# Performance work log

Measured on AMD Instinct MI355X. Metric: run time of the kernel, lower is better.

The kernel has to match this reference:

```python
import jax, jax.numpy as jnp
import numpy as np


def setup_inputs() -> dict:
    key = jax.random.key(0)
    k1, k2, k3 = jax.random.split(key, 3)
    B, F, D = 8192, 4096, 1024
    x = jax.random.normal(k1, (B, D), dtype=jnp.float32)
    mu = jax.random.normal(k2, (F, D), dtype=jnp.float32)
    # keep scales strictly positive and well-conditioned
    scale_diag = jax.random.uniform(k3, (F, D), dtype=jnp.float32, minval=0.5, maxval=1.5)
    return {"x": x, "mu": mu, "scale_diag": scale_diag}


def reference(x, mu, scale_diag):
    # Unnormalized diag-Gaussian log prob for every (batch, feature) pair:
    #   out[b, f] = sum_d -0.5 * ((x[b,d] - mu[f,d]) / scale[f,d])^2
    # Expanded to GEMM form (quadratic expansion):
    #   -0.5 * ( x^2 @ inv2.T  -  2 * x @ (mu*inv2).T  +  sum_d mu^2*inv2 )
    inv2 = 1.0 / (scale_diag * scale_diag)            # [F, D]
    xx = jnp.matmul(x * x, inv2.T)                    # [B, F]
    xm = jnp.matmul(x, (mu * inv2).T)                 # [B, F]
    mm = jnp.sum(mu * mu * inv2, axis=-1)             # [F]
    return -0.5 * (xx - 2.0 * xm + mm[None, :])       # [B, F]
```

## Files before the change

### kernel.cpp

```cpp
#include <hip/hip_runtime.h>
#include <hip/hip_bf16.h>
#include <cstdint>

#define B_SZ 8192
#define F_SZ 4096
#define D_SZ 1024
#define K_SZ 2048

typedef __bf16 bf16x8 __attribute__((ext_vector_type(8)));
typedef float f32x4 __attribute__((ext_vector_type(4)));
typedef float fvec4 __attribute__((ext_vector_type(4)));
typedef unsigned short u16x4 __attribute__((ext_vector_type(4)));

__device__ __forceinline__ unsigned short f2bf(float f) {
    union { float f; unsigned u; } c; c.f = f;
    unsigned r = c.u + 0x7fff + ((c.u >> 16) & 1);
    return (unsigned short)(r >> 16);
}

__device__ __forceinline__ void async16(const void* g, void* l) {
    __builtin_amdgcn_global_load_lds(
        (__attribute__((address_space(1))) void*)g,
        (__attribute__((address_space(3))) void*)l, 16, 0, 0);
}

__global__ __launch_bounds__(256) void prep(const float* __restrict__ x,
                                            const float* __restrict__ mu,
                                            const float* __restrict__ sd,
                                            unsigned short* __restrict__ A,
                                            unsigned short* __restrict__ W,
                                            float* __restrict__ nmm) {
    const int tid = threadIdx.x;
    if (blockIdx.x < 4096) {
        const size_t o0 = (size_t)blockIdx.x * 2048 + tid * 4;
        fvec4 v0 = *(const fvec4*)(x + o0);
        fvec4 v1 = *(const fvec4*)(x + o0 + 1024);
        #pragma unroll
        for (int h = 0; h < 2; ++h) {
            fvec4 v = h ? v1 : v0;
            size_t oo = o0 + h * 1024;
            size_t b = oo >> 10;
            int d = (int)(oo & 1023);
            u16x4 xx, xs;
            xx.x = f2bf(v.x * v.x); xx.y = f2bf(v.y * v.y);
            xx.z = f2bf(v.z * v.z); xx.w = f2bf(v.w * v.w);
            xs.x = f2bf(v.x); xs.y = f2bf(v.y);
            xs.z = f2bf(v.z); xs.w = f2bf(v.w);
            *(u16x4*)(A + b * K_SZ + d) = xx;
            *(u16x4*)(A + b * K_SZ + 1024 + d) = xs;
        }
    } else {
        const int f = blockIdx.x - 4096;
        const int d = tid * 4;
        size_t off = (size_t)f * D_SZ + d;
        fvec4 m = *(const fvec4*)(mu + off);
        fvec4 s = *(const fvec4*)(sd + off);
        float i0 = 1.0f / (s.x * s.x), i1 = 1.0f / (s.y * s.y);
        float i2 = 1.0f / (s.z * s.z), i3 = 1.0f / (s.w * s.w);
        u16x4 wi, wm;
        wi.x = f2bf(i0); wi.y = f2bf(i1); wi.z = f2bf(i2); wi.w = f2bf(i3);
        wm.x = f2bf(-2.0f * m.x * i0); wm.y = f2bf(-2.0f * m.y * i1);
        wm.z = f2bf(-2.0f * m.z * i2); wm.w = f2bf(-2.0f * m.w * i3);
        size_t wb = (size_t)f * K_SZ + d;
        *(u16x4*)(W + wb) = wi;
        *(u16x4*)(W + wb + 1024) = wm;
        float mm = m.x * m.x * i0 + m.y * m.y * i1 + m.z * m.z * i2 + m.w * m.w * i3;
        #pragma unroll
        for (int o = 32; o > 0; o >>= 1) mm += __shfl_down(mm, o, 64);
        __shared__ float red[4];
        if ((tid & 63) == 0) red[tid >> 6] = mm;
        __syncthreads();
        if (tid == 0) nmm[f] = -0.5f * (red[0] + red[1] + red[2] + red[3]);
    }
}

__global__ __launch_bounds__(256) void gemm_bt(const unsigned short* __restrict__ A,
                                               const unsigned short* __restrict__ W,
                                               const float* __restrict__ nmm,
                                               float* __restrict__ out) {
    __shared__ __align__(16) unsigned short sA[128 * 32];
    __shared__ __align__(16) unsigned short sB[128 * 32];

    const int tid  = threadIdx.x;
    const int wave = tid >> 6;
    const int lane = tid & 63;
    const int wm = (wave >> 1) * 64;
    const int wn = (wave & 1) * 64;
    const int tileM = blockIdx.y * 128;
    const int tileN = blockIdx.x * 128;
    const int r16  = lane & 15;
    const int quad = lane >> 4;

    const int row0 = tid >> 2;
    const int col0 = (tid & 3) * 8;
    unsigned short* ldsA0 = sA + (wave * 64) * 8;
    unsigned short* ldsA1 = sA + (256 + wave * 64) * 8;
    unsigned short* ldsB0 = sB + (wave * 64) * 8;
    unsigned short* ldsB1 = sB + (256 + wave * 64) * 8;

    const f32x4 vzero = {0.f, 0.f, 0.f, 0.f};
    f32x4 acc[4][4];
    #pragma unroll
    for (int i = 0; i < 4; ++i)
        #pragma unroll
        for (int j = 0; j < 4; ++j) acc[i][j] = vzero;

    for (int k0 = 0; k0 < K_SZ; k0 += 32) {
        async16(A + (size_t)(tileM + row0) * K_SZ + k0 + col0, ldsA0);
        async16(A + (size_t)(tileM + row0 + 64) * K_SZ + k0 + col0, ldsA1);
        async16(W + (size_t)(tileN + row0) * K_SZ + k0 + col0, ldsB0);
        async16(W + (size_t)(tileN + row0 + 64) * K_SZ + k0 + col0, ldsB1);
        __syncthreads();

        bf16x8 af[4], bfr[4];
        #pragma unroll
        for (int i = 0; i < 4; ++i)
            af[i] = *(const bf16x8*)(sA + (wm + i * 16 + r16) * 32 + quad * 8);
        #pragma unroll
        for (int j = 0; j < 4; ++j)
            bfr[j] = *(const bf16x8*)(sB + (wn + j * 16 + r16) * 32 + quad * 8);
        #pragma unroll
        for (int i = 0; i < 4; ++i)
            #pragma unroll
            for (int j = 0; j < 4; ++j)
                acc[i][j] = __builtin_amdgcn_mfma_f32_16x16x32_bf16(
                    af[i], bfr[j], acc[i][j], 0, 0, 0);
        __syncthreads();
    }

    int   fc[4];
    float cj[4];
    #pragma unroll
    for (int j = 0; j < 4; ++j) {
        fc[j] = tileN + wn + j * 16 + r16;
        cj[j] = nmm[fc[j]];
    }
    #pragma unroll
    for (int i = 0; i < 4; ++i) {
        int mbase = tileM + wm + i * 16 + quad * 4;
        #pragma unroll
        for (int r = 0; r < 4; ++r) {
            float* orow = out + (size_t)(mbase + r) * F_SZ;
            #pragma unroll
            for (int j = 0; j < 4; ++j)
                orow[fc[j]] = -0.5f * acc[i][j][r] + cj[j];
        }
    }
}

extern "C" void kernel_launch(void* const* d_in, const int* in_sizes, int n_in,
                              void* d_out, int out_size, void* d_ws, size_t ws_size,
                              hipStream_t stream) {
    const float* x  = (const float*)d_in[0];
    const float* mu = (const float*)d_in[1];
    const float* sd = (const float*)d_in[2];
    float* out = (float*)d_out;

    unsigned short* A = (unsigned short*)d_ws;
    unsigned short* W = A + (size_t)B_SZ * K_SZ;
    float* nmm = (float*)(W + (size_t)F_SZ * K_SZ);

    prep<<<8192, 256, 0, stream>>>(x, mu, sd, A, W, nmm);
    gemm_bt<<<dim3(F_SZ / 128, B_SZ / 128), 256, 0, stream>>>(A, W, nmm, out);
}
```

Baseline: 325.8 us.

## Warp-specialize GEMM with producer waves feeding a 4-stage LDS ring

Replaces the single-buffered, barrier-synchronized GEMM loop with a producer/consumer design. Two extra producer waves issue async global-to-LDS loads into a 4-stage ring. They signal readiness through LDS flags after vmcnt waits, and the four compute waves spin on those flags and acknowledge consumption with atomics. It also XOR-swizzles the LDS layout to reduce bank conflicts. The aim is to overlap memory latency with MFMA work, at the cost of spin-wait overhead, more LDS use (lower occupancy), and fragile hand-written vmcnt synchronization.

After: 379.7 us. +16.5%, slower.

```diff
diff --git a/kernel.cpp b/kernel.cpp
--- a/kernel.cpp
+++ b/kernel.cpp
@@ -74,29 +74,76 @@
     }
 }
 
-__global__ __launch_bounds__(256) void gemm_bt(const unsigned short* __restrict__ A,
+#define STAGES 4
+__global__ __launch_bounds__(384) void gemm_pc(const unsigned short* __restrict__ A,
                                                const unsigned short* __restrict__ W,
                                                const float* __restrict__ nmm,
                                                float* __restrict__ out) {
-    __shared__ __align__(16) unsigned short sA[128 * 32];
-    __shared__ __align__(16) unsigned short sB[128 * 32];
+    __shared__ __align__(16) unsigned short ring[STAGES][2][128 * 32];
+    __shared__ int flagA[STAGES];
+    __shared__ int flagB[STAGES];
+    __shared__ int consd[STAGES];
 
     const int tid  = threadIdx.x;
     const int wave = tid >> 6;
     const int lane = tid & 63;
+    const int tileM = blockIdx.y * 128;
+    const int tileN = blockIdx.x * 128;
+
+    if (tid < STAGES) { flagA[tid] = 0; flagB[tid] = 0; consd[tid] = 0; }
+    __syncthreads();
+
+    if (wave >= 4) {
+        const int part = wave - 4;
+        const unsigned short* src =
+            part == 0 ? A + (size_t)tileM * K_SZ : W + (size_t)tileN * K_SZ;
+        int* flg = part == 0 ? flagA : flagB;
+        const int lrow = lane >> 2;
+        const int cswz = (lane & 3) ^ ((lane >> 3) & 3);
+        const size_t laneoff = (size_t)lrow * K_SZ + cswz * 8;
+
+        auto issue = [&](int j) {
+            const int s = j & (STAGES - 1);
+            unsigned short* dst = &ring[s][part][0];
+            const size_t k0 = (size_t)j * 32;
+            #pragma unroll
+            for (int q = 0; q < 8; ++q)
+                async16(src + (size_t)q * 16 * K_SZ + laneoff + k0, dst + q * 512);
+        };
+        auto signal = [&](int s, int val, int pend) {
+            unsigned faddr = (unsigned)(uintptr_t)(&flg[s]);
+            if (pend == 16)
+                asm volatile("s_waitcnt vmcnt(16)\n\tds_write_b32 %0, %1\n"
+                             :: "v"(faddr), "v"(val) : "memory");
+            else if (pend == 8)
+                asm volatile("s_waitcnt vmcnt(8)\n\tds_write_b32 %0, %1\n"
+                             :: "v"(faddr), "v"(val) : "memory");
+            else
+                asm volatile("s_waitcnt vmcnt(0)\n\tds_write_b32 %0, %1\n"
+                             :: "v"(faddr), "v"(val) : "memory");
+        };
+
+        issue(0); issue(1); issue(2);
+        for (int i = 0; i <= 61; ++i) {
+            signal(i & (STAGES - 1), i + 1, 16);
+            const int j = i + 3;
+            if (j < 64) {
+                const int s = j & (STAGES - 1), w = j >> 2;
+                while (((volatile int*)consd)[s] < 4 * w) {}
+                asm volatile("" ::: "memory");
+                issue(j);
+            }
+        }
+        signal(62 & 3, 63, 8);
+        signal(63 & 3, 64, 0);
+        return;
+    }
+
     const int wm = (wave >> 1) * 64;
     const int wn = (wave & 1) * 64;
-    const int tileM = blockIdx.y * 128;
-    const int tileN = blockIdx.x * 128;
     const int r16  = lane & 15;
     const int quad = lane >> 4;
-
-    const int row0 = tid >> 2;
-    const int col0 = (tid & 3) * 8;
-    unsigned short* ldsA0 = sA + (wave * 64) * 8;
-    unsigned short* ldsA1 = sA + (256 + wave * 64) * 8;
-    unsigned short* ldsB0 = sB + (wave * 64) * 8;
-    unsigned short* ldsB1 = sB + (256 + wave * 64) * 8;
+    const int swz  = (r16 >> 1) & 3;
 
     const f32x4 vzero = {0.f, 0.f, 0.f, 0.f};
     f32x4 acc[4][4];
@@ -105,27 +152,30 @@
         #pragma unroll
         for (int j = 0; j < 4; ++j) acc[i][j] = vzero;
 
-    for (int k0 = 0; k0 < K_SZ; k0 += 32) {
-        async16(A + (size_t)(tileM + row0) * K_SZ + k0 + col0, ldsA0);
-        async16(A + (size_t)(tileM + row0 + 64) * K_SZ + k0 + col0, ldsA1);
-        async16(W + (size_t)(tileN + row0) * K_SZ + k0 + col0, ldsB0);
-        async16(W + (size_t)(tileN + row0 + 64) * K_SZ + k0 + col0, ldsB1);
-        __syncthreads();
-
+    for (int it = 0; it < 64; ++it) {
+        const int s = it & (STAGES - 1);
+        while (((volatile int*)flagA)[s] < it + 1 ||
+               ((volatile int*)flagB)[s] < it + 1) {}
+        asm volatile("" ::: "memory");
+
+        const unsigned short* tA = &ring[s][0][0];
+        const unsigned short* tB = &ring[s][1][0];
         bf16x8 af[4], bfr[4];
         #pragma unroll
         for (int i = 0; i < 4; ++i)
-            af[i] = *(const bf16x8*)(sA + (wm + i * 16 + r16) * 32 + quad * 8);
+            af[i] = *(const bf16x8*)(tA + (wm + i * 16 + r16) * 32 + (quad ^ swz) * 8);
         #pragma unroll
         for (int j = 0; j < 4; ++j)
-            bfr[j] = *(const bf16x8*)(sB + (wn + j * 16 + r16) * 32 + quad * 8);
+            bfr[j] = *(const bf16x8*)(tB + (wn + j * 16 + r16) * 32 + (quad ^ swz) * 8);
         #pragma unroll
         for (int i = 0; i < 4; ++i)
             #pragma unroll
             for (int j = 0; j < 4; ++j)
                 acc[i][j] = __builtin_amdgcn_mfma_f32_16x16x32_bf16(
                     af[i], bfr[j], acc[i][j], 0, 0, 0);
-        __syncthreads();
+
+        asm volatile("" ::: "memory");
+        if (lane == 0) atomicAdd(&consd[s], 1);
     }
 
     int   fc[4];
@@ -161,5 +211,5 @@
     float* nmm = (float*)(W + (size_t)F_SZ * K_SZ);
 
     prep<<<8192, 256, 0, stream>>>(x, mu, sd, A, W, nmm);
-    gemm_bt<<<dim3(F_SZ / 128, B_SZ / 128), 256, 0, stream>>>(A, W, nmm, out);
-}
+    gemm_pc<<<dim3(F_SZ / 128, B_SZ / 128), 384, 0, stream>>>(A, W, nmm, out);
+}
```
